# Performance work log

Measured on AMD Instinct MI355X. Metric: run time of the kernel, lower is better.

## Reference

```python
import jax, jax.numpy as jnp
import numpy as np

B, S, D = 4, 4096, 256

def setup_inputs() -> dict:
    key = jax.random.key(0)
    ks = jax.random.split(key, 7)
    s = 1.0 / np.sqrt(D)
    return {
        "x": jax.random.normal(ks[0], (B, S, D), dtype=jnp.float32),
        "Wq": jax.random.uniform(ks[1], (D, D), jnp.float32, -s, s),
        "bq": jax.random.uniform(ks[2], (D,), jnp.float32, -s, s),
        "Wk": jax.random.uniform(ks[3], (D, D), jnp.float32, -s, s),
        "bk": jax.random.uniform(ks[4], (D,), jnp.float32, -s, s),
        "Wv": jax.random.uniform(ks[5], (D, D), jnp.float32, -s, s),
        "bv": jax.random.uniform(ks[6], (D,), jnp.float32, -s, s),
    }

def reference(x, Wq, bq, Wk, bk, Wv, bv):
    q = x @ Wq + bq            # [B,S,D]
    k = x @ Wk + bk
    v = x @ Wv + bv
    scores = jnp.einsum('bqd,bkd->bqk', q, k) / jnp.sqrt(jnp.float32(D))
    attn = jax.nn.softmax(scores, axis=-1)  # [B,S,S]
    return jnp.einsum('bqk,bkd->bqd', attn, v)
```

## Files before the change

### kernel.cpp

```cpp
#include <hip/hip_runtime.h>

typedef short v8s __attribute__((ext_vector_type(8)));
typedef float v4f __attribute__((ext_vector_type(4)));
typedef unsigned short u16;
typedef unsigned int u32;
typedef u16 v4u __attribute__((ext_vector_type(4)));

#define SS 4096
#define DD 256
#define QB 128
#define KVB 32

__device__ __forceinline__ u16 f2bf(float f) {
  u32 u = __builtin_bit_cast(u32, f);
  return (u16)((u + 0x7FFFu + ((u >> 16) & 1u)) >> 16);
}

__device__ __forceinline__ void gload16(const u16* g, u16* l) {
  __builtin_amdgcn_global_load_lds((const __attribute__((address_space(1))) u32*)g,
                                   (__attribute__((address_space(3))) u32*)l, 16, 0, 0);
}

__global__ void wcast_kernel(const float* __restrict__ Wq, const float* __restrict__ Wk,
                             const float* __restrict__ Wv, u16* __restrict__ wt) {
  int f = blockIdx.x * 256 + threadIdx.x;
  int p = f >> 16, rem = f & 65535, n = rem >> 8, k = rem & 255;
  const float* W = (p == 0) ? Wq : ((p == 1) ? Wk : Wv);
  wt[f] = f2bf(W[k * 256 + n]);
}

__global__ __launch_bounds__(256) void proj_kernel(
    const float* __restrict__ x, const u16* __restrict__ wt,
    const float* __restrict__ bq, const float* __restrict__ bk, const float* __restrict__ bv,
    u16* __restrict__ qg, u16* __restrict__ kg, u16* __restrict__ vtg) {
  __shared__ u16 xs[64 * 256];
  const int tid = threadIdx.x;
  const int lane = tid & 63, w = tid >> 6, g = lane >> 4, l15 = lane & 15;
  const int tok0 = blockIdx.x * 64;

#pragma unroll
  for (int it = 0; it < 8; ++it) {
    int idx = it * 256 + tid;
    int r = idx >> 5, d0 = (idx & 31) << 3;
    const float* src = x + (size_t)(tok0 + r) * DD + d0;
    float4 a = *(const float4*)src;
    float4 bb = *(const float4*)(src + 4);
    v8s pk;
    pk[0] = (short)f2bf(a.x);  pk[1] = (short)f2bf(a.y);
    pk[2] = (short)f2bf(a.z);  pk[3] = (short)f2bf(a.w);
    pk[4] = (short)f2bf(bb.x); pk[5] = (short)f2bf(bb.y);
    pk[6] = (short)f2bf(bb.z); pk[7] = (short)f2bf(bb.w);
    *(v8s*)(xs + r * DD + (((d0 >> 3) ^ (r & 7)) << 3)) = pk;
  }
  __syncthreads();

  v8s af[4][8];
#pragma unroll
  for (int m = 0; m < 4; ++m) {
    const int row = 16 * m + l15;
#pragma unroll
    for (int c = 0; c < 8; ++c)
      af[m][c] = *(const v8s*)(xs + row * DD + ((((4 * c + g) ^ (row & 7))) << 3));
  }

  const float SCL = 0.0625f * 1.44269504088896f;
  for (int p = 0; p < 3; ++p) {
    const u16* wbase = wt + p * 65536;
    const float* bias = (p == 0) ? bq : ((p == 1) ? bk : bv);
    v4f acc[4][4];
    const v4f vzero = {0.f, 0.f, 0.f, 0.f};
#pragma unroll
    for (int m = 0; m < 4; ++m)
#pragma unroll
      for (int t = 0; t < 4; ++t) acc[m][t] = vzero;
#pragma unroll
    for (int t = 0; t < 4; ++t) {
      const int n = 64 * w + 16 * t + l15;
      const u16* wrow = wbase + n * 256;
#pragma unroll
      for (int c = 0; c < 8; ++c) {
        v8s bf = *(const v8s*)(wrow + 8 * g + 32 * c);
#pragma unroll
        for (int m = 0; m < 4; ++m)
          acc[m][t] = __builtin_amdgcn_mfma_f32_16x16x32_bf16(af[m][c], bf, acc[m][t], 0, 0, 0);
      }
    }
    if (p == 0) {
#pragma unroll
      for (int t = 0; t < 4; ++t) {
        int n = 64 * w + 16 * t + l15;
        float bb = bias[n];
#pragma unroll
        for (int m = 0; m < 4; ++m)
#pragma unroll
          for (int r = 0; r < 4; ++r)
            qg[(size_t)(tok0 + 16 * m + 4 * g + r) * DD + n] = f2bf((acc[m][t][r] + bb) * SCL);
      }
    } else if (p == 1) {
#pragma unroll
      for (int t = 0; t < 4; ++t) {
        int n = 64 * w + 16 * t + l15;
        float bb = bias[n];
#pragma unroll
        for (int m = 0; m < 4; ++m)
#pragma unroll
          for (int r = 0; r < 4; ++r)
            kg[(size_t)(tok0 + 16 * m + 4 * g + r) * DD + n] = f2bf(acc[m][t][r] + bb);
      }
    } else {
      const int b = tok0 >> 12;
      const int s0 = tok0 & 4095;
#pragma unroll
      for (int t = 0; t < 4; ++t) {
        int n = 64 * w + 16 * t + l15;
        float bb = bias[n];
#pragma unroll
        for (int m = 0; m < 4; ++m) {
          v4u pk;
#pragma unroll
          for (int r = 0; r < 4; ++r) pk[r] = f2bf(acc[m][t][r] + bb);
          *(v4u*)(vtg + (size_t)(b * DD + n) * SS + s0 + 16 * m + 4 * g) = pk;
        }
      }
    }
  }
}

#define STAGE(kt_, buf_)                                                          \
  {                                                                               \
    const int kt__ = (kt_);                                                       \
    u16* kd = kb + (buf_)*8192;                                                   \
    u16* vd = vt + (buf_)*8192;                                                   \
    _Pragma("unroll")                                                             \
    for (int it = 0; it < 4; ++it) {                                              \
      int idx = it * 256 + tid;                                                   \
      int r = idx >> 5, db = idx & 31;                                            \
      gload16(kbase + (size_t)(kt__ * KVB + r) * DD + ((db ^ (r & 7)) << 3),      \
              kd + idx * 8);                                                      \
    }                                                                             \
    _Pragma("unroll")                                                             \
    for (int it = 0; it < 4; ++it) {                                              \
      int idx = it * 256 + tid;                                                   \
      int d = idx >> 2, jb = idx & 3;                                             \
      gload16(vbase + (size_t)d * SS + kt__ * KVB + (((jb ^ (d >> 1)) & 3) << 3), \
              vd + idx * 8);                                                      \
    }                                                                             \
  }

__global__ __attribute__((amdgpu_flat_work_group_size(256, 256),
                          amdgpu_waves_per_eu(2))) void attn_kernel(
    const u16* __restrict__ qg, const u16* __restrict__ kg, const u16* __restrict__ vtg,
    float* __restrict__ o0, float* __restrict__ opart, float* __restrict__ ml,
    int nsplit, int nblk) {
  extern __shared__ u16 sm[];
  u16* kb = sm;
  u16* vt = sm + 16384;

  const int bid = blockIdx.x;
  const int lg = (bid & 7) * (nblk >> 3) + (bid >> 3);
  const int slice = lg >> 7;
  const int rem = lg & 127;
  const int b = rem >> 5;
  const int qt = rem & 31;
  const int NT = (SS / KVB) / nsplit;
  const int koff = slice * (SS / nsplit);

  const int tid = threadIdx.x;
  const int lane = tid & 63, w = tid >> 6, g = lane >> 4, l15 = lane & 15;

  const u16* qbase = qg + (size_t)(b * SS + qt * QB) * DD;
  const u16* kbase = kg + (size_t)(b * SS + koff) * DD;
  const u16* vbase = vtg + (size_t)b * DD * SS + koff;

  STAGE(0, 0);

  v8s qf[2][8];
#pragma unroll
  for (int j = 0; j < 2; ++j) {
    const u16* qr = qbase + (size_t)(32 * w + 16 * j + l15) * DD;
#pragma unroll
    for (int c = 0; c < 8; ++c)
      qf[j][c] = *(const v8s*)(qr + ((4 * c + g) << 3));
  }

  float mrow[2], lrow[2];
  v4f oacc[2][16];
  const v4f vzero = {0.f, 0.f, 0.f, 0.f};
#pragma unroll
  for (int j = 0; j < 2; ++j) { mrow[j] = -1e30f; lrow[j] = 0.f; }
#pragma unroll
  for (int m = 0; m < 2; ++m)
#pragma unroll
    for (int t = 0; t < 16; ++t) oacc[m][t] = vzero;

  for (int kt = 0; kt < NT; ++kt) {
    const int cur = kt & 1;
    __syncthreads();
    if (kt + 1 < NT) STAGE(kt + 1, cur ^ 1);
    const u16* kc = kb + cur * 8192;
    const u16* vc = vt + cur * 8192;

    v4f sacc[2][2];
#pragma unroll
    for (int t = 0; t < 2; ++t)
#pragma unroll
      for (int j = 0; j < 2; ++j) sacc[t][j] = vzero;
    __builtin_amdgcn_s_setprio(1);
#pragma unroll
    for (int c = 0; c < 8; ++c) {
#pragma unroll
      for (int t = 0; t < 2; ++t) {
        const int krow = 16 * t + l15;
        v8s kf = *(const v8s*)(kc + krow * DD + ((((4 * c + g) ^ (krow & 7))) << 3));
#pragma unroll
        for (int j = 0; j < 2; ++j)
          sacc[t][j] = __builtin_amdgcn_mfma_f32_16x16x32_bf16(kf, qf[j][c], sacc[t][j], 0, 0, 0);
      }
    }
    __builtin_amdgcn_s_setprio(0);

    float tml[2];
#pragma unroll
    for (int j = 0; j < 2; ++j) {
      float a0 = fmaxf(fmaxf(sacc[0][j][0], sacc[0][j][1]), fmaxf(sacc[0][j][2], sacc[0][j][3]));
      float a1 = fmaxf(fmaxf(sacc[1][j][0], sacc[1][j][1]), fmaxf(sacc[1][j][2], sacc[1][j][3]));
      tml[j] = fmaxf(a0, a1);
    }
    const bool ok = (tml[0] - mrow[0] <= 11.0f) && (tml[1] - mrow[1] <= 11.0f);
    if (!__all(ok)) {
      float sc[2];
#pragma unroll
      for (int j = 0; j < 2; ++j) {
        float t0 = fmaxf(tml[j], __shfl_xor(tml[j], 16));
        t0 = fmaxf(t0, __shfl_xor(t0, 32));
        float nm = fmaxf(mrow[j], t0);
        sc[j] = exp2f(mrow[j] - nm);
        mrow[j] = nm;
        lrow[j] *= sc[j];
      }
#pragma unroll
      for (int m = 0; m < 2; ++m) {
#pragma unroll
        for (int r = 0; r < 4; ++r) {
          float s4 = __shfl(sc[m], (lane & 48) | (4 * g + r));
#pragma unroll
          for (int t = 0; t < 16; ++t) oacc[m][t][r] *= s4;
        }
      }
    }

    v8s pa[2];
#pragma unroll
    for (int j = 0; j < 2; ++j) {
      u32 m32[4];
      float ls = 0.f;
#pragma unroll
      for (int t = 0; t < 2; ++t) {
        float e0 = exp2f(sacc[t][j][0] - mrow[j]);
        float e1 = exp2f(sacc[t][j][1] - mrow[j]);
        float e2 = exp2f(sacc[t][j][2] - mrow[j]);
        float e3 = exp2f(sacc[t][j][3] - mrow[j]);
        ls += (e0 + e1) + (e2 + e3);
        u32 lo, hi;
        asm("v_cvt_pk_bf16_f32 %0, %1, %2" : "=v"(lo) : "v"(e0), "v"(e1));
        asm("v_cvt_pk_bf16_f32 %0, %1, %2" : "=v"(hi) : "v"(e2), "v"(e3));
        m32[2 * t] = lo;
        m32[2 * t + 1] = hi;
      }
      lrow[j] += ls;
      const int la = l15 | ((g & 1) << 5);
      const int lb = la + 16;
      u32 A0 = (u32)__shfl((int)m32[0], la), A2 = (u32)__shfl((int)m32[2], la);
      u32 B1 = (u32)__shfl((int)m32[1], la), B3 = (u32)__shfl((int)m32[3], la);
      u32 C0 = (u32)__shfl((int)m32[0], lb), C2 = (u32)__shfl((int)m32[2], lb);
      u32 D1 = (u32)__shfl((int)m32[1], lb), D3 = (u32)__shfl((int)m32[3], lb);
      const bool sel = ((g >> 1) & 1) != 0;
      union { v8s v; u32 u[4]; } P;
      P.u[0] = sel ? A2 : A0;
      P.u[1] = sel ? B3 : B1;
      P.u[2] = sel ? C2 : C0;
      P.u[3] = sel ? D3 : D1;
      pa[j] = P.v;
    }

    __builtin_amdgcn_s_setprio(1);
#pragma unroll
    for (int t = 0; t < 16; ++t) {
      const int d = 16 * t + l15;
      v8s bvv = *(const v8s*)(vc + d * KVB + (((g ^ (d >> 1)) & 3) << 3));
#pragma unroll
      for (int m = 0; m < 2; ++m)
        oacc[m][t] = __builtin_amdgcn_mfma_f32_16x16x32_bf16(pa[m], bvv, oacc[m][t], 0, 0, 0);
    }
    __builtin_amdgcn_s_setprio(0);
  }

#pragma unroll
  for (int j = 0; j < 2; ++j) {
    lrow[j] += __shfl_xor(lrow[j], 16);
    lrow[j] += __shfl_xor(lrow[j], 32);
  }
  float* ob = (slice == 0) ? o0 : (opart + (size_t)(slice - 1) * 4194304);
  const size_t rb = (size_t)b * SS + (size_t)qt * QB;
  if (g == 0) {
#pragma unroll
    for (int j = 0; j < 2; ++j) {
      const size_t rowg = rb + 32 * w + 16 * j + l15;
      float2 v2 = make_float2(mrow[j], lrow[j]);
      *(float2*)(ml + ((size_t)slice * 16384 + rowg) * 2) = v2;
    }
  }
#pragma unroll
  for (int m = 0; m < 2; ++m)
#pragma unroll
    for (int t = 0; t < 16; ++t)
#pragma unroll
      for (int r = 0; r < 4; ++r)
        ob[(rb + 32 * w + 16 * m + 4 * g + r) * DD + 16 * t + l15] = oacc[m][t][r];
}

__global__ __launch_bounds__(256) void combine_kernel(
    float* __restrict__ out, const float* __restrict__ opart,
    const float* __restrict__ ml, int nsplit) {
  const int tid = threadIdx.x;
  const size_t row = (size_t)blockIdx.x * 4 + (tid >> 6);
  const int d = (tid & 63) * 4;
  float2 mls[4];
  float mm = -1e30f;
#pragma unroll
  for (int s = 0; s < 4; ++s) {
    if (s < nsplit) {
      mls[s] = *(const float2*)(ml + ((size_t)s * 16384 + row) * 2);
      mm = fmaxf(mm, mls[s].x);
    }
  }
  float l = 0.f;
  float4 acc = {0.f, 0.f, 0.f, 0.f};
#pragma unroll
  for (int s = 0; s < 4; ++s) {
    if (s < nsplit) {
      float a = exp2f(mls[s].x - mm);
      const float* src = (s == 0) ? (out + row * DD + d)
                                  : (opart + (size_t)(s - 1) * 4194304 + row * DD + d);
      float4 v = *(const float4*)src;
      l += a * mls[s].y;
      acc.x += a * v.x; acc.y += a * v.y; acc.z += a * v.z; acc.w += a * v.w;
    }
  }
  float inv = 1.0f / l;
  acc.x *= inv; acc.y *= inv; acc.z *= inv; acc.w *= inv;
  *(float4*)(out + row * DD + d) = acc;
}

extern "C" void kernel_launch(void* const* d_in, const int* in_sizes, int n_in,
                              void* d_out, int out_size, void* d_ws, size_t ws_size,
                              hipStream_t stream) {
  const float* x  = (const float*)d_in[0];
  const float* Wq = (const float*)d_in[1];
  const float* bq = (const float*)d_in[2];
  const float* Wk = (const float*)d_in[3];
  const float* bk = (const float*)d_in[4];
  const float* Wv = (const float*)d_in[5];
  const float* bv = (const float*)d_in[6];
  float* out = (float*)d_out;
  char* ws = (char*)d_ws;

  u16* wt    = (u16*)ws;
  u16* qg    = (u16*)(ws + 393216);
  u16* kg    = (u16*)(ws + 393216 + 8388608);
  u16* vtg   = (u16*)(ws + 393216 + 2 * 8388608);
  float* ml  = (float*)(ws + 25559040);
  float* op  = (float*)(ws + 26083328);
  const size_t need4 = 26083328ull + 3ull * 16777216ull;
  const size_t need2 = 26083328ull + 1ull * 16777216ull;
  const int nsplit = (ws_size >= need4) ? 4 : ((ws_size >= need2) ? 2 : 1);
  const int nblk = 128 * nsplit;

  (void)hipFuncSetAttribute((const void*)attn_kernel,
                            hipFuncAttributeMaxDynamicSharedMemorySize, 65536);

  wcast_kernel<<<dim3(768), dim3(256), 0, stream>>>(Wq, Wk, Wv, wt);
  proj_kernel<<<dim3(256), dim3(256), 0, stream>>>(x, wt, bq, bk, bv, qg, kg, vtg);
  attn_kernel<<<dim3(nblk), dim3(256), 65536, stream>>>(qg, kg, vtg, out, op, ml, nsplit, nblk);
  combine_kernel<<<dim3(4096), dim3(256), 0, stream>>>(out, op, ml, nsplit);
}
```

Measured before the change: 167.0 us.

## Software-pipeline QK of next tile with PV of current tile; stream second Q fragment

Restructures the attention loop so that the QK^T MFMAs for tile kt+1 are issued alongside the PV MFMAs for tile kt. The softmax for the next tile then runs after PV, so matrix and ALU work from different tiles can overlap. K staging now runs two tiles ahead and V staging one tile ahead. Only the first Q fragment stays in registers; the second is reloaded from global memory on every step to free registers. The cost is extra global/L2 traffic for Q and more complex buffer sequencing.

New measurement: 204.1 us. 22.2% more time.

```diff
diff --git a/kernel.cpp b/kernel.cpp
--- a/kernel.cpp
+++ b/kernel.cpp
@@ -126,11 +126,10 @@
   }
 }
 
-#define STAGE(kt_, buf_)                                                          \
+#define STAGE_K(kt_, buf_)                                                        \
   {                                                                               \
     const int kt__ = (kt_);                                                       \
     u16* kd = kb + (buf_)*8192;                                                   \
-    u16* vd = vt + (buf_)*8192;                                                   \
     _Pragma("unroll")                                                             \
     for (int it = 0; it < 4; ++it) {                                              \
       int idx = it * 256 + tid;                                                   \
@@ -138,12 +137,102 @@
       gload16(kbase + (size_t)(kt__ * KVB + r) * DD + ((db ^ (r & 7)) << 3),      \
               kd + idx * 8);                                                      \
     }                                                                             \
+  }
+
+#define STAGE_V(kt_, buf_)                                                        \
+  {                                                                               \
+    const int kt__ = (kt_);                                                       \
+    u16* vd = vt + (buf_)*8192;                                                   \
     _Pragma("unroll")                                                             \
     for (int it = 0; it < 4; ++it) {                                              \
       int idx = it * 256 + tid;                                                   \
       int d = idx >> 2, jb = idx & 3;                                             \
       gload16(vbase + (size_t)d * SS + kt__ * KVB + (((jb ^ (d >> 1)) & 3) << 3), \
               vd + idx * 8);                                                      \
+    }                                                                             \
+  }
+
+#define QKSTEP(S, KC)                                                             \
+  {                                                                               \
+    const u16* q1 = qr1base;                                                      \
+    asm volatile("" : "+v"(q1));                                                  \
+    __builtin_amdgcn_s_setprio(1);                                                \
+    _Pragma("unroll")                                                             \
+    for (int c = 0; c < 8; ++c) {                                                 \
+      v8s q1f = *(const v8s*)(q1 + ((4 * c + g) << 3));                           \
+      _Pragma("unroll")                                                           \
+      for (int t = 0; t < 2; ++t) {                                               \
+        const int krow = 16 * t + l15;                                            \
+        v8s kf = *(const v8s*)((KC) + krow * DD + ((((4 * c + g) ^ (krow & 7))) << 3)); \
+        S[t][0] = __builtin_amdgcn_mfma_f32_16x16x32_bf16(kf, qf0[c], S[t][0], 0, 0, 0); \
+        S[t][1] = __builtin_amdgcn_mfma_f32_16x16x32_bf16(kf, q1f, S[t][1], 0, 0, 0);    \
+      }                                                                           \
+    }                                                                             \
+    __builtin_amdgcn_s_setprio(0);                                                \
+  }
+
+#define SOFTMAX(S)                                                                \
+  {                                                                               \
+    float tml[2];                                                                 \
+    _Pragma("unroll")                                                             \
+    for (int j = 0; j < 2; ++j) {                                                 \
+      float a0 = fmaxf(fmaxf(S[0][j][0], S[0][j][1]), fmaxf(S[0][j][2], S[0][j][3])); \
+      float a1 = fmaxf(fmaxf(S[1][j][0], S[1][j][1]), fmaxf(S[1][j][2], S[1][j][3])); \
+      tml[j] = fmaxf(a0, a1);                                                     \
+    }                                                                             \
+    const bool ok = (tml[0] - mrow[0] <= 11.0f) && (tml[1] - mrow[1] <= 11.0f);   \
+    if (!__all(ok)) {                                                             \
+      float sc[2];                                                                \
+      _Pragma("unroll")                                                           \
+      for (int j = 0; j < 2; ++j) {                                               \
+        float t0 = fmaxf(tml[j], __shfl_xor(tml[j], 16));                         \
+        t0 = fmaxf(t0, __shfl_xor(t0, 32));                                       \
+        float nm = fmaxf(mrow[j], t0);                                            \
+        sc[j] = exp2f(mrow[j] - nm);                                              \
+        mrow[j] = nm;                                                             \
+        lrow[j] *= sc[j];                                                         \
+      }                                                                           \
+      _Pragma("unroll")                                                           \
+      for (int m_ = 0; m_ < 2; ++m_) {                                            \
+        _Pragma("unroll")                                                         \
+        for (int r_ = 0; r_ < 4; ++r_) {                                          \
+          float s4 = __shfl(sc[m_], (lane & 48) | (4 * g + r_));                  \
+          _Pragma("unroll")                                                       \
+          for (int t_ = 0; t_ < 16; ++t_) oacc[m_][t_][r_] *= s4;                 \
+        }                                                                         \
+      }                                                                           \
+    }                                                                             \
+    _Pragma("unroll")                                                             \
+    for (int j = 0; j < 2; ++j) {                                                 \
+      u32 m32[4];                                                                 \
+      float ls = 0.f;                                                             \
+      _Pragma("unroll")                                                           \
+      for (int t_ = 0; t_ < 2; ++t_) {                                            \
+        float e0 = exp2f(S[t_][j][0] - mrow[j]);                                  \
+        float e1 = exp2f(S[t_][j][1] - mrow[j]);                                  \
+        float e2 = exp2f(S[t_][j][2] - mrow[j]);                                  \
+        float e3 = exp2f(S[t_][j][3] - mrow[j]);                                  \
+        ls += (e0 + e1) + (e2 + e3);                                              \
+        u32 lo, hi;                                                               \
+        asm("v_cvt_pk_bf16_f32 %0, %1, %2" : "=v"(lo) : "v"(e0), "v"(e1));        \
+        asm("v_cvt_pk_bf16_f32 %0, %1, %2" : "=v"(hi) : "v"(e2), "v"(e3));        \
+        m32[2 * t_] = lo;                                                         \
+        m32[2 * t_ + 1] = hi;                                                     \
+      }                                                                           \
+      lrow[j] += ls;                                                              \
+      const int la = l15 | ((g & 1) << 5);                                        \
+      const int lb = la + 16;                                                     \
+      u32 A0 = (u32)__shfl((int)m32[0], la), A2 = (u32)__shfl((int)m32[2], la);   \
+      u32 B1 = (u32)__shfl((int)m32[1], la), B3 = (u32)__shfl((int)m32[3], la);   \
+      u32 C0 = (u32)__shfl((int)m32[0], lb), C2 = (u32)__shfl((int)m32[2], lb);   \
+      u32 D1 = (u32)__shfl((int)m32[1], lb), D3 = (u32)__shfl((int)m32[3], lb);   \
+      const bool sel = ((g >> 1) & 1) != 0;                                       \
+      union { v8s v; u32 u[4]; } P;                                               \
+      P.u[0] = sel ? A2 : A0;                                                     \
+      P.u[1] = sel ? B3 : B1;                                                     \
+      P.u[2] = sel ? C2 : C0;                                                     \
+      P.u[3] = sel ? D3 : D1;                                                     \
+      pa[j] = P.v;                                                                \
     }                                                                             \
   }
 
@@ -172,16 +261,16 @@
   const u16* kbase = kg + (size_t)(b * SS + koff) * DD;
   const u16* vbase = vtg + (size_t)b * DD * SS + koff;
 
-  STAGE(0, 0);
-
-  v8s qf[2][8];
-#pragma unroll
-  for (int j = 0; j < 2; ++j) {
-    const u16* qr = qbase + (size_t)(32 * w + 16 * j + l15) * DD;
-#pragma unroll
-    for (int c = 0; c < 8; ++c)
-      qf[j][c] = *(const v8s*)(qr + ((4 * c + g) << 3));
-  }
+  STAGE_K(0, 0);
+  STAGE_V(0, 0);
+
+  v8s qf0[8];
+  {
+    const u16* qr0 = qbase + (size_t)(32 * w + l15) * DD;
+#pragma unroll
+    for (int c = 0; c < 8; ++c) qf0[c] = *(const v8s*)(qr0 + ((4 * c + g) << 3));
+  }
+  const u16* qr1base = qbase + (size_t)(32 * w + 16 + l15) * DD;
 
   float mrow[2], lrow[2];
   v4f oacc[2][16];
@@ -193,106 +282,51 @@
 #pragma unroll
     for (int t = 0; t < 16; ++t) oacc[m][t] = vzero;
 
+  __syncthreads();
+  if (NT > 1) STAGE_K(1, 1);
+
+  v8s pa[2];
+  {
+    v4f sacc[2][2];
+#pragma unroll
+    for (int t = 0; t < 2; ++t)
+#pragma unroll
+      for (int j = 0; j < 2; ++j) sacc[t][j] = vzero;
+    QKSTEP(sacc, kb);
+    SOFTMAX(sacc);
+  }
+
   for (int kt = 0; kt < NT; ++kt) {
     const int cur = kt & 1;
     __syncthreads();
-    if (kt + 1 < NT) STAGE(kt + 1, cur ^ 1);
-    const u16* kc = kb + cur * 8192;
-    const u16* vc = vt + cur * 8192;
+    const bool more = (kt + 1 < NT);
+    if (kt + 2 < NT) STAGE_K(kt + 2, cur);
+    if (more) STAGE_V(kt + 1, cur ^ 1);
 
     v4f sacc[2][2];
 #pragma unroll
     for (int t = 0; t < 2; ++t)
 #pragma unroll
       for (int j = 0; j < 2; ++j) sacc[t][j] = vzero;
-    __builtin_amdgcn_s_setprio(1);
-#pragma unroll
-    for (int c = 0; c < 8; ++c) {
-#pragma unroll
-      for (int t = 0; t < 2; ++t) {
-        const int krow = 16 * t + l15;
-        v8s kf = *(const v8s*)(kc + krow * DD + ((((4 * c + g) ^ (krow & 7))) << 3));
-#pragma unroll
-        for (int j = 0; j < 2; ++j)
-          sacc[t][j] = __builtin_amdgcn_mfma_f32_16x16x32_bf16(kf, qf[j][c], sacc[t][j], 0, 0, 0);
+    if (more) {
+      const u16* kc = kb + (cur ^ 1) * 8192;
+      QKSTEP(sacc, kc);
+    }
+
+    {
+      const u16* vc = vt + cur * 8192;
+      __builtin_amdgcn_s_setprio(1);
+#pragma unroll
+      for (int t = 0; t < 16; ++t) {
+        const int d = 16 * t + l15;
+        v8s bvv = *(const v8s*)(vc + d * KVB + (((g ^ (d >> 1)) & 3) << 3));
+        oacc[0][t] = __builtin_amdgcn_mfma_f32_16x16x32_bf16(pa[0], bvv, oacc[0][t], 0, 0, 0);
+        oacc[1][t] = __builtin_amdgcn_mfma_f32_16x16x32_bf16(pa[1], bvv, oacc[1][t], 0, 0, 0);
       }
-    }
-    __builtin_amdgcn_s_setprio(0);
-
-    float tml[2];
-#pragma unroll
-    for (int j = 0; j < 2; ++j) {
-      float a0 = fmaxf(fmaxf(sacc[0][j][0], sacc[0][j][1]), fmaxf(sacc[0][j][2], sacc[0][j][3]));
-      float a1 = fmaxf(fmaxf(sacc[1][j][0], sacc[1][j][1]), fmaxf(sacc[1][j][2], sacc[1][j][3]));
-      tml[j] = fmaxf(a0, a1);
-    }
-    const bool ok = (tml[0] - mrow[0] <= 11.0f) && (tml[1] - mrow[1] <= 11.0f);
-    if (!__all(ok)) {
-      float sc[2];
-#pragma unroll
-      for (int j = 0; j < 2; ++j) {
-        float t0 = fmaxf(tml[j], __shfl_xor(tml[j], 16));
-        t0 = fmaxf(t0, __shfl_xor(t0, 32));
-        float nm = fmaxf(mrow[j], t0);
-        sc[j] = exp2f(mrow[j] - nm);
-        mrow[j] = nm;
-        lrow[j] *= sc[j];
-      }
-#pragma unroll
-      for (int m = 0; m < 2; ++m) {
-#pragma unroll
-        for (int r = 0; r < 4; ++r) {
-          float s4 = __shfl(sc[m], (lane & 48) | (4 * g + r));
-#pragma unroll
-          for (int t = 0; t < 16; ++t) oacc[m][t][r] *= s4;
-        }
-      }
-    }
-
-    v8s pa[2];
-#pragma unroll
-    for (int j = 0; j < 2; ++j) {
-      u32 m32[4];
-      float ls = 0.f;
-#pragma unroll
-      for (int t = 0; t < 2; ++t) {
-        float e0 = exp2f(sacc[t][j][0] - mrow[j]);
-        float e1 = exp2f(sacc[t][j][1] - mrow[j]);
-        float e2 = exp2f(sacc[t][j][2] - mrow[j]);
-        float e3 = exp2f(sacc[t][j][3] - mrow[j]);
-        ls += (e0 + e1) + (e2 + e3);
-        u32 lo, hi;
-        asm("v_cvt_pk_bf16_f32 %0, %1, %2" : "=v"(lo) : "v"(e0), "v"(e1));
-        asm("v_cvt_pk_bf16_f32 %0, %1, %2" : "=v"(hi) : "v"(e2), "v"(e3));
-        m32[2 * t] = lo;
-        m32[2 * t + 1] = hi;
-      }
-      lrow[j] += ls;
-      const int la = l15 | ((g & 1) << 5);
-      const int lb = la + 16;
-      u32 A0 = (u32)__shfl((int)m32[0], la), A2 = (u32)__shfl((int)m32[2], la);
-      u32 B1 = (u32)__shfl((int)m32[1], la), B3 = (u32)__shfl((int)m32[3], la);
-      u32 C0 = (u32)__shfl((int)m32[0], lb), C2 = (u32)__shfl((int)m32[2], lb);
-      u32 D1 = (u32)__shfl((int)m32[1], lb), D3 = (u32)__shfl((int)m32[3], lb);
-      const bool sel = ((g >> 1) & 1) != 0;
-      union { v8s v; u32 u[4]; } P;
-      P.u[0] = sel ? A2 : A0;
-      P.u[1] = sel ? B3 : B1;
-      P.u[2] = sel ? C2 : C0;
-      P.u[3] = sel ? D3 : D1;
-      pa[j] = P.v;
-    }
-
-    __builtin_amdgcn_s_setprio(1);
-#pragma unroll
-    for (int t = 0; t < 16; ++t) {
-      const int d = 16 * t + l15;
-      v8s bvv = *(const v8s*)(vc + d * KVB + (((g ^ (d >> 1)) & 3) << 3));
-#pragma unroll
-      for (int m = 0; m < 2; ++m)
-        oacc[m][t] = __builtin_amdgcn_mfma_f32_16x16x32_bf16(pa[m], bvv, oacc[m][t], 0, 0, 0);
-    }
-    __builtin_amdgcn_s_setprio(0);
+      __builtin_amdgcn_s_setprio(0);
+    }
+
+    if (more) SOFTMAX(sacc);
   }
 
 #pragma unroll
```
